# Kernel optimization log

Measured on AMD Instinct MI355X. Metric: run time of the kernel, lower is better.

Reference implementation:

```python
import jax, jax.numpy as jnp
import numpy as np

M, K, N = 4096, 4096, 4096

def setup_inputs() -> dict:
    key = jax.random.key(0)
    k1, k2, k3 = jax.random.split(key, 3)
    a = jax.random.randint(k1, (M, K), 0, 127, dtype=jnp.int32)
    b = jax.random.randint(k2, (K, N), 0, 127, dtype=jnp.int32)
    scale = jax.random.uniform(k3, (N,), dtype=jnp.float32)
    return {"a": a, "b": b, "scale": scale}

def reference(a, b, scale):
    a8 = a.astype(jnp.int8)
    b8 = b.astype(jnp.int8)
    acc = jnp.matmul(a8, b8, preferred_element_type=jnp.int32)  # [M, N] int32
    # fused per-column (per-output-channel) dequantization scale
    return acc.astype(jnp.float32) * scale[None, :]  # [M, N] float32
```

## Files before the change

### kernel.cpp

```cpp
#include <hip/hip_runtime.h>
#include <stdint.h>

#define M_DIM 4096
#define K_DIM 4096
#define N_DIM 4096

typedef int v4i __attribute__((ext_vector_type(4)));
typedef int int32x4 __attribute__((ext_vector_type(4)));

__device__ __forceinline__ void gload_lds16(const void* g, void* l) {
    __builtin_amdgcn_global_load_lds(
        (const __attribute__((address_space(1))) uint32_t*)g,
        (__attribute__((address_space(3))) uint32_t*)l, 16, 0, 0);
}

__global__ void pack_ab_kernel(const int* __restrict__ a, char* __restrict__ a8,
                               const int* __restrict__ b, char* __restrict__ b8t) {
    __shared__ char tile[64][68];
    if (blockIdx.x < 2048) {
        int idx = blockIdx.x * 256 + threadIdx.x;
        const int stride = 2048 * 256;
        const int total4 = M_DIM * K_DIM / 4;
        for (int i = idx; i < total4; i += stride) {
            int32x4 v = ((const int32x4*)a)[i];
            uint32_t p = (uint32_t)(v.x & 0xff) | ((uint32_t)(v.y & 0xff) << 8) |
                         ((uint32_t)(v.z & 0xff) << 16) | ((uint32_t)(v.w & 0xff) << 24);
            ((uint32_t*)a8)[i] = p;
        }
    } else {
        int bid2 = blockIdx.x - 2048;
        int n0 = (bid2 & 63) * 64;
        int k0 = (bid2 >> 6) * 64;
        int tx = threadIdx.x & 63;
        int ty = threadIdx.x >> 6;
#pragma unroll
        for (int kk = 0; kk < 64; kk += 4) {
            tile[kk + ty][tx] = (char)b[(size_t)(k0 + kk + ty) * N_DIM + n0 + tx];
        }
        __syncthreads();
        int td = threadIdx.x & 15;
        int tn = threadIdx.x >> 4;
#pragma unroll
        for (int nn0 = 0; nn0 < 64; nn0 += 16) {
            int nn = nn0 + tn;
            uint32_t p = (uint32_t)(uint8_t)tile[td * 4 + 0][nn] |
                         ((uint32_t)(uint8_t)tile[td * 4 + 1][nn] << 8) |
                         ((uint32_t)(uint8_t)tile[td * 4 + 2][nn] << 16) |
                         ((uint32_t)(uint8_t)tile[td * 4 + 3][nn] << 24);
            *(uint32_t*)&b8t[(size_t)(n0 + nn) * K_DIM + k0 + td * 4] = p;
        }
    }
}

#define BM 256
#define BN 256
#define KTILES (K_DIM / 64)

#define BAR __builtin_amdgcn_s_barrier()
#define WAIT_VM4 asm volatile("s_waitcnt vmcnt(4)" ::: "memory")
#define WAIT_VM0 asm volatile("s_waitcnt vmcnt(0)" ::: "memory")
#define WAIT_LGKM0 asm volatile("s_waitcnt lgkmcnt(0)" ::: "memory")

#define RD_FRAGS(RA, RB)                                                                \
    _Pragma("unroll") for (int i_ = 0; i_ < 8; ++i_)                                    \
        RA[i_] = *(const v4i*)(lds + nxt + aOff + i_ * 1024);                           \
    _Pragma("unroll") for (int j_ = 0; j_ < 4; ++j_)                                    \
        RB[j_] = *(const v4i*)(lds + nxt + bOff + j_ * 1024);

#define SGB_HINT                                                                        \
    _Pragma("unroll") for (int g_ = 0; g_ < 12; ++g_) {                                 \
        __builtin_amdgcn_sched_group_barrier(0x100, 1, 0);               \
        __builtin_amdgcn_sched_group_barrier(0x008, 2, 0);                  \
    }                                                                                   \
    __builtin_amdgcn_sched_group_barrier(0x008, 8, 0);

#define MFMA32(AF, BF)                                                                  \
    __builtin_amdgcn_s_setprio(1);                                                      \
    _Pragma("unroll") for (int i_ = 0; i_ < 8; ++i_)                                    \
    _Pragma("unroll") for (int j_ = 0; j_ < 4; ++j_)                                    \
        acc[i_][j_] = __builtin_amdgcn_mfma_i32_16x16x64_i8(AF[i_], BF[j_],             \
                                                            acc[i_][j_], 0, 0, 0);     \
    __builtin_amdgcn_s_setprio(0);

#define WINDOW(w, RA, RB, MA, MB)                                                       \
    {                                                                                   \
        stage((w) + 2, stg);                                                            \
        WAIT_VM4;                                                                       \
        BAR;                                                                            \
        RD_FRAGS(RA, RB);                                                               \
        SGB_HINT;                                                                       \
        MFMA32(MA, MB);                                                                 \
        WAIT_LGKM0;                                                                     \
        int t_ = cur; cur = nxt; nxt = stg; stg = t_;                                   \
    }

__global__ __launch_bounds__(512, 2) void gemm_i8_pp(const char* __restrict__ A8,
                                                     const char* __restrict__ B8T,
                                                     const float* __restrict__ scale,
                                                     float* __restrict__ out) {
    __shared__ char lds[98304];

    int tid = threadIdx.x;
    int wave = tid >> 6;
    int lane = tid & 63;
    int wr = wave >> 2;
    int wc = wave & 3;
    int l15 = lane & 15;

    int bid = blockIdx.x;
    int swz = (bid & 7) * 32 + (bid >> 3);
    int bm = swz >> 4;
    int bn = swz & 15;

    int rA = tid >> 2;
    int cc = ((tid & 3) ^ ((tid >> 3) & 3)) << 4;
    const char* aSrc = A8 + (size_t)(bm * BM + rA) * K_DIM + cc;
    const char* bSrc = B8T + (size_t)(bn * BN + rA) * K_DIM + cc;

    int slot = (((lane >> 4) ^ ((lane >> 1) & 3)) << 4);
    int aOff = wr * 8192 + l15 * 64 + slot;
    int bOff = 16384 + wc * 4096 + l15 * 64 + slot;

    v4i acc[8][4];
#pragma unroll
    for (int i = 0; i < 8; ++i)
#pragma unroll
        for (int j = 0; j < 4; ++j) acc[i][j] = (v4i){0, 0, 0, 0};

    auto stage = [&](int w, int bo) {
        const char* sa = aSrc + (size_t)w * 64;
        const char* sb = bSrc + (size_t)w * 64;
        char* da = (char*)lds + bo + wave * 1024;
        char* db = da + 16384;
        gload_lds16(sa, da);
        gload_lds16(sa + (size_t)128 * K_DIM, da + 8192);
        gload_lds16(sb, db);
        gload_lds16(sb + (size_t)128 * K_DIM, db + 8192);
    };

    stage(0, 0);
    stage(1, 32768);
    WAIT_VM4;
    BAR;

    int cur = 0, nxt = 32768, stg = 65536;
    v4i pA[8], pB[4], qA[8], qB[4];
    {
#pragma unroll
        for (int i = 0; i < 8; ++i) pA[i] = *(const v4i*)(lds + cur + aOff + i * 1024);
#pragma unroll
        for (int j = 0; j < 4; ++j) pB[j] = *(const v4i*)(lds + cur + bOff + j * 1024);
    }

    for (int kt = 0; kt < KTILES - 2; kt += 2) {
        WINDOW(kt, qA, qB, pA, pB);
        WINDOW(kt + 1, pA, pB, qA, qB);
    }

    WAIT_VM0;
    BAR;
    RD_FRAGS(qA, qB);
    MFMA32(pA, pB);
    MFMA32(qA, qB);

    size_t orow0 = (size_t)bm * BM + wr * 128 + (lane >> 4) * 4;
    int ocol0 = bn * BN + wc * 64 + l15;
#pragma unroll
    for (int j = 0; j < 4; ++j) {
        int col = ocol0 + j * 16;
        float s = scale[col];
#pragma unroll
        for (int i = 0; i < 8; ++i) {
            size_t row = orow0 + (size_t)i * 16;
#pragma unroll
            for (int r = 0; r < 4; ++r) {
                out[(row + r) * N_DIM + col] = (float)acc[i][j][r] * s;
            }
        }
    }
}

#define FBM 128
#define FBN 128
#define FBK 64

__global__ __launch_bounds__(256) void gemm_i8_fused_kernel(const int* __restrict__ a,
                                                            const int* __restrict__ b,
                                                            const float* __restrict__ scale,
                                                            float* __restrict__ out) {
    __shared__ char As[FBM * FBK];
    __shared__ char Bs[FBN * FBK];

    int tid = threadIdx.x;
    int wave = tid >> 6;
    int lane = tid & 63;

    int nwg = gridDim.x;
    int cpx = nwg >> 3;
    int bid = blockIdx.x;
    int swz = (bid & 7) * cpx + (bid >> 3);
    int bm = swz >> 5;
    int bn = swz & 31;

    int f0 = tid * 16;
    int m0 = f0 >> 6;
    int k0 = f0 & 63;

    int nn = tid & 127;
    int kh = tid >> 7;

    int wr = wave >> 1;
    int wc = wave & 1;
    int lrow = lane & 15;
    int kgrp = (lane >> 4) * 16;

    v4i acc[4][4];
#pragma unroll
    for (int i = 0; i < 4; ++i)
#pragma unroll
        for (int j = 0; j < 4; ++j) acc[i][j] = (v4i){0, 0, 0, 0};

    const int kTiles = K_DIM / FBK;
    for (int kt = 0; kt < kTiles; ++kt) {
        __syncthreads();
#pragma unroll
        for (int r = 0; r < 2; ++r) {
            const int* src = a + (size_t)(bm * FBM + m0 + r * 64) * K_DIM + kt * FBK + k0;
            uint32_t pk[4];
#pragma unroll
            for (int q = 0; q < 4; ++q) {
                int32x4 v = *(const int32x4*)(src + q * 4);
                pk[q] = (uint32_t)(v.x & 0xff) | ((uint32_t)(v.y & 0xff) << 8) |
                        ((uint32_t)(v.z & 0xff) << 16) | ((uint32_t)(v.w & 0xff) << 24);
            }
            *(v4i*)&As[f0 + r * 4096] = (v4i){(int)pk[0], (int)pk[1], (int)pk[2], (int)pk[3]};
        }
#pragma unroll
        for (int d = 0; d < 8; ++d) {
            uint32_t p = 0;
#pragma unroll
            for (int i = 0; i < 4; ++i) {
                int kk = kt * FBK + kh * 32 + d * 4 + i;
                p |= (uint32_t)(b[(size_t)kk * N_DIM + bn * FBN + nn] & 0xff) << (8 * i);
            }
            *(uint32_t*)&Bs[nn * 64 + kh * 32 + d * 4] = p;
        }
        __syncthreads();

        v4i aF[4], bF[4];
#pragma unroll
        for (int i = 0; i < 4; ++i)
            aF[i] = *(const v4i*)&As[(wr * 64 + i * 16 + lrow) * FBK + kgrp];
#pragma unroll
        for (int j = 0; j < 4; ++j)
            bF[j] = *(const v4i*)&Bs[(wc * 64 + j * 16 + lrow) * FBK + kgrp];
#pragma unroll
        for (int i = 0; i < 4; ++i)
#pragma unroll
            for (int j = 0; j < 4; ++j)
                acc[i][j] = __builtin_amdgcn_mfma_i32_16x16x64_i8(aF[i], bF[j], acc[i][j], 0, 0, 0);
    }

    size_t orow0 = (size_t)bm * FBM + wr * 64;
    int ocol0 = bn * FBN + wc * 64;
#pragma unroll
    for (int j = 0; j < 4; ++j) {
        int col = ocol0 + j * 16 + lrow;
        float s = scale[col];
#pragma unroll
        for (int i = 0; i < 4; ++i) {
            size_t row = orow0 + i * 16 + (lane >> 4) * 4;
#pragma unroll
            for (int r = 0; r < 4; ++r) {
                out[(row + r) * N_DIM + col] = (float)acc[i][j][r] * s;
            }
        }
    }
}

extern "C" void kernel_launch(void* const* d_in, const int* in_sizes, int n_in,
                              void* d_out, int out_size, void* d_ws, size_t ws_size,
                              hipStream_t stream) {
    const int* a = (const int*)d_in[0];
    const int* b = (const int*)d_in[1];
    const float* scale = (const float*)d_in[2];
    float* out = (float*)d_out;

    size_t need = (size_t)M_DIM * K_DIM + (size_t)K_DIM * N_DIM;
    if (ws_size >= need) {
        char* a8 = (char*)d_ws;
        char* b8t = a8 + (size_t)M_DIM * K_DIM;
        pack_ab_kernel<<<2048 + 4096, 256, 0, stream>>>(a, a8, b, b8t);
        gemm_i8_pp<<<256, 512, 0, stream>>>(a8, b8t, scale, out);
    } else {
        gemm_i8_fused_kernel<<<1024, 256, 0, stream>>>(a, b, scale, out);
    }
}
```

Before: 93.30 us.

## Load B fragments directly from global into registers, stage only A in LDS

B operand fragments now go straight from global memory into registers one k-tile ahead, so B no longer passes through LDS. This halves the LDS footprint and removes the LDS reads for B. The wait counts and scheduling hints are retuned to match, and the block swizzle swaps bm and bn. In exchange, each B fragment is a 16-byte strided load straight from HBM/L2 with no LDS reuse across the waves that share the same columns, which may raise global traffic and latency exposure.

```diff
diff --git a/kernel.cpp b/kernel.cpp
--- a/kernel.cpp
+++ b/kernel.cpp
@@ -57,20 +57,20 @@
 #define KTILES (K_DIM / 64)
 
 #define BAR __builtin_amdgcn_s_barrier()
+#define WAIT_VM6 asm volatile("s_waitcnt vmcnt(6)" ::: "memory")
 #define WAIT_VM4 asm volatile("s_waitcnt vmcnt(4)" ::: "memory")
+#define WAIT_VM2 asm volatile("s_waitcnt vmcnt(2)" ::: "memory")
 #define WAIT_VM0 asm volatile("s_waitcnt vmcnt(0)" ::: "memory")
 #define WAIT_LGKM0 asm volatile("s_waitcnt lgkmcnt(0)" ::: "memory")
 
-#define RD_FRAGS(RA, RB)                                                                \
+#define RD_A(RA)                                                                        \
     _Pragma("unroll") for (int i_ = 0; i_ < 8; ++i_)                                    \
-        RA[i_] = *(const v4i*)(lds + nxt + aOff + i_ * 1024);                           \
-    _Pragma("unroll") for (int j_ = 0; j_ < 4; ++j_)                                    \
-        RB[j_] = *(const v4i*)(lds + nxt + bOff + j_ * 1024);
+        RA[i_] = *(const v4i*)(lds + nxt + aOff + i_ * 1024);
 
 #define SGB_HINT                                                                        \
-    _Pragma("unroll") for (int g_ = 0; g_ < 12; ++g_) {                                 \
+    _Pragma("unroll") for (int g_ = 0; g_ < 8; ++g_) {                                  \
         __builtin_amdgcn_sched_group_barrier(0x100, 1, 0);               \
-        __builtin_amdgcn_sched_group_barrier(0x008, 2, 0);                  \
+        __builtin_amdgcn_sched_group_barrier(0x008, 3, 0);                  \
     }                                                                                   \
     __builtin_amdgcn_sched_group_barrier(0x008, 8, 0);
 
@@ -82,23 +82,24 @@
                                                             acc[i_][j_], 0, 0, 0);     \
     __builtin_amdgcn_s_setprio(0);
 
-#define WINDOW(w, RA, RB, MA, MB)                                                       \
+#define WINDOW(w, LA, LB, UA, UB)                                                       \
     {                                                                                   \
+        loadB((w) + 1, LB);                                                             \
         stage((w) + 2, stg);                                                            \
-        WAIT_VM4;                                                                       \
+        WAIT_VM6;                                                                       \
         BAR;                                                                            \
-        RD_FRAGS(RA, RB);                                                               \
+        RD_A(LA);                                                                       \
         SGB_HINT;                                                                       \
-        MFMA32(MA, MB);                                                                 \
+        MFMA32(UA, UB);                                                                 \
         WAIT_LGKM0;                                                                     \
         int t_ = cur; cur = nxt; nxt = stg; stg = t_;                                   \
     }
 
-__global__ __launch_bounds__(512, 2) void gemm_i8_pp(const char* __restrict__ A8,
+__global__ __launch_bounds__(512, 2) void gemm_i8_bd(const char* __restrict__ A8,
                                                      const char* __restrict__ B8T,
                                                      const float* __restrict__ scale,
                                                      float* __restrict__ out) {
-    __shared__ char lds[98304];
+    __shared__ char lds[49152];
 
     int tid = threadIdx.x;
     int wave = tid >> 6;
@@ -109,17 +110,18 @@
 
     int bid = blockIdx.x;
     int swz = (bid & 7) * 32 + (bid >> 3);
-    int bm = swz >> 4;
-    int bn = swz & 15;
+    int bm = swz & 15;
+    int bn = swz >> 4;
 
     int rA = tid >> 2;
     int cc = ((tid & 3) ^ ((tid >> 3) & 3)) << 4;
     const char* aSrc = A8 + (size_t)(bm * BM + rA) * K_DIM + cc;
-    const char* bSrc = B8T + (size_t)(bn * BN + rA) * K_DIM + cc;
+
+    const char* bFragSrc =
+        B8T + (size_t)(bn * BN + wc * 64 + l15) * K_DIM + ((lane >> 4) << 4);
 
     int slot = (((lane >> 4) ^ ((lane >> 1) & 3)) << 4);
     int aOff = wr * 8192 + l15 * 64 + slot;
-    int bOff = 16384 + wc * 4096 + l15 * 64 + slot;
 
     v4i acc[8][4];
 #pragma unroll
@@ -129,38 +131,39 @@
 
     auto stage = [&](int w, int bo) {
         const char* sa = aSrc + (size_t)w * 64;
-        const char* sb = bSrc + (size_t)w * 64;
         char* da = (char*)lds + bo + wave * 1024;
-        char* db = da + 16384;
         gload_lds16(sa, da);
         gload_lds16(sa + (size_t)128 * K_DIM, da + 8192);
-        gload_lds16(sb, db);
-        gload_lds16(sb + (size_t)128 * K_DIM, db + 8192);
     };
+    auto loadB = [&](int w, v4i* dst) {
+#pragma unroll
+        for (int j = 0; j < 4; ++j)
+            dst[j] = *(const v4i*)(bFragSrc + (size_t)j * 16 * K_DIM + (size_t)w * 64);
+    };
+
+    v4i pA[8], qA[8], pB[4], qB[4];
 
     stage(0, 0);
-    stage(1, 32768);
-    WAIT_VM4;
+    loadB(0, pB);
+    stage(1, 16384);
+    WAIT_VM2;
     BAR;
-
-    int cur = 0, nxt = 32768, stg = 65536;
-    v4i pA[8], pB[4], qA[8], qB[4];
-    {
-#pragma unroll
-        for (int i = 0; i < 8; ++i) pA[i] = *(const v4i*)(lds + cur + aOff + i * 1024);
-#pragma unroll
-        for (int j = 0; j < 4; ++j) pB[j] = *(const v4i*)(lds + cur + bOff + j * 1024);
-    }
+#pragma unroll
+    for (int i = 0; i < 8; ++i) pA[i] = *(const v4i*)(lds + 0 + aOff + i * 1024);
+
+    int cur = 0, nxt = 16384, stg = 32768;
 
     for (int kt = 0; kt < KTILES - 2; kt += 2) {
         WINDOW(kt, qA, qB, pA, pB);
         WINDOW(kt + 1, pA, pB, qA, qB);
     }
 
+    loadB(63, qB);
+    WAIT_VM4;
+    BAR;
+    RD_A(qA);
+    MFMA32(pA, pB);
     WAIT_VM0;
-    BAR;
-    RD_FRAGS(qA, qB);
-    MFMA32(pA, pB);
     MFMA32(qA, qB);
 
     size_t orow0 = (size_t)bm * BM + wr * 128 + (lane >> 4) * 4;
@@ -291,7 +294,7 @@
         char* a8 = (char*)d_ws;
         char* b8t = a8 + (size_t)M_DIM * K_DIM;
         pack_ab_kernel<<<2048 + 4096, 256, 0, stream>>>(a, a8, b, b8t);
-        gemm_i8_pp<<<256, 512, 0, stream>>>(a8, b8t, scale, out);
+        gemm_i8_bd<<<256, 512, 0, stream>>>(a8, b8t, scale, out);
     } else {
         gemm_i8_fused_kernel<<<1024, 256, 0, stream>>>(a, b, scale, out);
     }
```

Result: slower. 115.6 us (+23.9%).

## Switch int8 GEMM to 128-wide K tiles with double-buffered LDS

Applied to the files above, without the earlier changes.

Replaces the triple-buffered 64-wide K pipeline with a double-buffered pipeline over 128-wide K tiles, using 128 KB of LDS. Each window issues eight global-to-LDS loads and 64 MFMAs, which halves the number of barriers and loop iterations per K. The LDS swizzle changes to an 8-chunk XOR on 128-byte rows, and the fragment reads are interleaved with MFMAs through a new sched_group_barrier pattern. The trade-off is less prefetch depth: only one tile is in flight instead of two, and a barrier has to be added before each stage. The larger LDS footprint may also cut residency to one block per CU instead of two.

```diff
diff --git a/kernel.cpp b/kernel.cpp
--- a/kernel.cpp
+++ b/kernel.cpp
@@ -54,25 +54,19 @@
 
 #define BM 256
 #define BN 256
-#define KTILES (K_DIM / 64)
+#define KTILES (K_DIM / 128)
 
 #define BAR __builtin_amdgcn_s_barrier()
-#define WAIT_VM4 asm volatile("s_waitcnt vmcnt(4)" ::: "memory")
+#define WAIT_VM8 asm volatile("s_waitcnt vmcnt(8)" ::: "memory")
 #define WAIT_VM0 asm volatile("s_waitcnt vmcnt(0)" ::: "memory")
-#define WAIT_LGKM0 asm volatile("s_waitcnt lgkmcnt(0)" ::: "memory")
-
-#define RD_FRAGS(RA, RB)                                                                \
-    _Pragma("unroll") for (int i_ = 0; i_ < 8; ++i_)                                    \
-        RA[i_] = *(const v4i*)(lds + nxt + aOff + i_ * 1024);                           \
-    _Pragma("unroll") for (int j_ = 0; j_ < 4; ++j_)                                    \
-        RB[j_] = *(const v4i*)(lds + nxt + bOff + j_ * 1024);
-
-#define SGB_HINT                                                                        \
-    _Pragma("unroll") for (int g_ = 0; g_ < 12; ++g_) {                                 \
-        __builtin_amdgcn_sched_group_barrier(0x100, 1, 0);               \
-        __builtin_amdgcn_sched_group_barrier(0x008, 2, 0);                  \
+
+#define SGB_W128                                                                        \
+    __builtin_amdgcn_sched_group_barrier(0x100, 5, 0);                                  \
+    _Pragma("unroll") for (int g_ = 0; g_ < 19; ++g_) {                                 \
+        __builtin_amdgcn_sched_group_barrier(0x100, 1, 0);                              \
+        __builtin_amdgcn_sched_group_barrier(0x008, 3, 0);                              \
     }                                                                                   \
-    __builtin_amdgcn_sched_group_barrier(0x008, 8, 0);
+    __builtin_amdgcn_sched_group_barrier(0x008, 7, 0);
 
 #define MFMA32(AF, BF)                                                                  \
     __builtin_amdgcn_s_setprio(1);                                                      \
@@ -82,23 +76,26 @@
                                                             acc[i_][j_], 0, 0, 0);     \
     __builtin_amdgcn_s_setprio(0);
 
-#define WINDOW(w, RA, RB, MA, MB)                                                       \
+#define COMPUTE_WIN(cur)                                                                \
     {                                                                                   \
-        stage((w) + 2, stg);                                                            \
-        WAIT_VM4;                                                                       \
-        BAR;                                                                            \
-        RD_FRAGS(RA, RB);                                                               \
-        SGB_HINT;                                                                       \
-        MFMA32(MA, MB);                                                                 \
-        WAIT_LGKM0;                                                                     \
-        int t_ = cur; cur = nxt; nxt = stg; stg = t_;                                   \
-    }
-
-__global__ __launch_bounds__(512, 2) void gemm_i8_pp(const char* __restrict__ A8,
-                                                     const char* __restrict__ B8T,
-                                                     const float* __restrict__ scale,
-                                                     float* __restrict__ out) {
-    __shared__ char lds[98304];
+        _Pragma("unroll") for (int j_ = 0; j_ < 4; ++j_)                                \
+            fB0[j_] = *(const v4i*)(lds + (cur) + bBase + j_ * 2048);                   \
+        _Pragma("unroll") for (int i_ = 0; i_ < 8; ++i_)                                \
+            fA0[i_] = *(const v4i*)(lds + (cur) + aBase + i_ * 2048);                   \
+        _Pragma("unroll") for (int j_ = 0; j_ < 4; ++j_)                                \
+            fB1[j_] = *(const v4i*)(lds + (cur) + ((bBase + j_ * 2048) ^ 64));          \
+        _Pragma("unroll") for (int i_ = 0; i_ < 8; ++i_)                                \
+            fA1[i_] = *(const v4i*)(lds + (cur) + ((aBase + i_ * 2048) ^ 64));          \
+        SGB_W128;                                                                       \
+        MFMA32(fA0, fB0);                                                               \
+        MFMA32(fA1, fB1);                                                               \
+    }
+
+__global__ __launch_bounds__(512, 2) void gemm_i8_w128(const char* __restrict__ A8,
+                                                       const char* __restrict__ B8T,
+                                                       const float* __restrict__ scale,
+                                                       float* __restrict__ out) {
+    __shared__ char lds[131072];
 
     int tid = threadIdx.x;
     int wave = tid >> 6;
@@ -106,20 +103,21 @@
     int wr = wave >> 2;
     int wc = wave & 3;
     int l15 = lane & 15;
+    int q = lane >> 4;
 
     int bid = blockIdx.x;
     int swz = (bid & 7) * 32 + (bid >> 3);
     int bm = swz >> 4;
     int bn = swz & 15;
 
-    int rA = tid >> 2;
-    int cc = ((tid & 3) ^ ((tid >> 3) & 3)) << 4;
-    const char* aSrc = A8 + (size_t)(bm * BM + rA) * K_DIM + cc;
-    const char* bSrc = B8T + (size_t)(bn * BN + rA) * K_DIM + cc;
-
-    int slot = (((lane >> 4) ^ ((lane >> 1) & 3)) << 4);
-    int aOff = wr * 8192 + l15 * 64 + slot;
-    int bOff = 16384 + wc * 4096 + l15 * 64 + slot;
+    int sRow = tid >> 3;
+    int sCh = ((tid & 7) ^ (sRow & 7)) << 4;
+    const char* aSrc = A8 + (size_t)(bm * BM + sRow) * K_DIM + sCh;
+    const char* bSrc = B8T + (size_t)(bn * BN + sRow) * K_DIM + sCh;
+
+    int slot0 = ((q ^ (l15 & 7)) << 4);
+    int aBase = (wr * 128 + l15) * 128 + slot0;
+    int bBase = 32768 + (wc * 64 + l15) * 128 + slot0;
 
     v4i acc[8][4];
 #pragma unroll
@@ -128,40 +126,35 @@
         for (int j = 0; j < 4; ++j) acc[i][j] = (v4i){0, 0, 0, 0};
 
     auto stage = [&](int w, int bo) {
-        const char* sa = aSrc + (size_t)w * 64;
-        const char* sb = bSrc + (size_t)w * 64;
+        const char* sa = aSrc + (size_t)w * 128;
+        const char* sb = bSrc + (size_t)w * 128;
         char* da = (char*)lds + bo + wave * 1024;
-        char* db = da + 16384;
-        gload_lds16(sa, da);
-        gload_lds16(sa + (size_t)128 * K_DIM, da + 8192);
-        gload_lds16(sb, db);
-        gload_lds16(sb + (size_t)128 * K_DIM, db + 8192);
+#pragma unroll
+        for (int r = 0; r < 4; ++r) {
+            gload_lds16(sa + (size_t)r * 64 * K_DIM, da + r * 8192);
+            gload_lds16(sb + (size_t)r * 64 * K_DIM, da + 32768 + r * 8192);
+        }
     };
 
+    v4i fA0[8], fB0[4], fA1[8], fB1[4];
+
     stage(0, 0);
-    stage(1, 32768);
-    WAIT_VM4;
-    BAR;
-
-    int cur = 0, nxt = 32768, stg = 65536;
-    v4i pA[8], pB[4], qA[8], qB[4];
+
+    for (int w = 0; w < KTILES - 1; ++w) {
+        int cur = (w & 1) << 16;
+        BAR;
+        stage(w + 1, cur ^ 65536);
+        WAIT_VM8;
+        BAR;
+        COMPUTE_WIN(cur);
+    }
+
     {
-#pragma unroll
-        for (int i = 0; i < 8; ++i) pA[i] = *(const v4i*)(lds + cur + aOff + i * 1024);
-#pragma unroll
-        for (int j = 0; j < 4; ++j) pB[j] = *(const v4i*)(lds + cur + bOff + j * 1024);
-    }
-
-    for (int kt = 0; kt < KTILES - 2; kt += 2) {
-        WINDOW(kt, qA, qB, pA, pB);
-        WINDOW(kt + 1, pA, pB, qA, qB);
-    }
-
-    WAIT_VM0;
-    BAR;
-    RD_FRAGS(qA, qB);
-    MFMA32(pA, pB);
-    MFMA32(qA, qB);
+        int cur = ((KTILES - 1) & 1) << 16;
+        WAIT_VM0;
+        BAR;
+        COMPUTE_WIN(cur);
+    }
 
     size_t orow0 = (size_t)bm * BM + wr * 128 + (lane >> 4) * 4;
     int ocol0 = bn * BN + wc * 64 + l15;
@@ -291,7 +284,7 @@
         char* a8 = (char*)d_ws;
         char* b8t = a8 + (size_t)M_DIM * K_DIM;
         pack_ab_kernel<<<2048 + 4096, 256, 0, stream>>>(a, a8, b, b8t);
-        gemm_i8_pp<<<256, 512, 0, stream>>>(a8, b8t, scale, out);
+        gemm_i8_w128<<<256, 512, 0, stream>>>(a8, b8t, scale, out);
     } else {
         gemm_i8_fused_kernel<<<1024, 256, 0, stream>>>(a, b, scale, out);
     }
```

Result: slower. 97.05 us (+4.0%).

## Use 4 fat waves per block with 128x128 per-wave tiles instead of 8

Applied to the files above, without the earlier changes.

Restructures the int8 GEMM block from 8 waves (each 128x64 output) to 4 waves (each 128x128 output), doubling per-wave accumulators and B fragments and the MFMAs per window. Each thread now issues 8 global-to-LDS loads per stage, with the wait count and scheduling hints adjusted to match, and the priority toggling is dropped. The aim is more register-level reuse of LDS fragments and fewer LDS reads per MFMA. In exchange, registers per wave rise sharply and fewer waves are resident to hide latency.

```diff
diff --git a/kernel.cpp b/kernel.cpp
--- a/kernel.cpp
+++ b/kernel.cpp
@@ -57,54 +57,51 @@
 #define KTILES (K_DIM / 64)
 
 #define BAR __builtin_amdgcn_s_barrier()
-#define WAIT_VM4 asm volatile("s_waitcnt vmcnt(4)" ::: "memory")
+#define WAIT_VM8 asm volatile("s_waitcnt vmcnt(8)" ::: "memory")
 #define WAIT_VM0 asm volatile("s_waitcnt vmcnt(0)" ::: "memory")
 #define WAIT_LGKM0 asm volatile("s_waitcnt lgkmcnt(0)" ::: "memory")
 
 #define RD_FRAGS(RA, RB)                                                                \
     _Pragma("unroll") for (int i_ = 0; i_ < 8; ++i_)                                    \
         RA[i_] = *(const v4i*)(lds + nxt + aOff + i_ * 1024);                           \
-    _Pragma("unroll") for (int j_ = 0; j_ < 4; ++j_)                                    \
+    _Pragma("unroll") for (int j_ = 0; j_ < 8; ++j_)                                    \
         RB[j_] = *(const v4i*)(lds + nxt + bOff + j_ * 1024);
 
 #define SGB_HINT                                                                        \
-    _Pragma("unroll") for (int g_ = 0; g_ < 12; ++g_) {                                 \
+    _Pragma("unroll") for (int g_ = 0; g_ < 16; ++g_) {                                 \
         __builtin_amdgcn_sched_group_barrier(0x100, 1, 0);               \
-        __builtin_amdgcn_sched_group_barrier(0x008, 2, 0);                  \
-    }                                                                                   \
-    __builtin_amdgcn_sched_group_barrier(0x008, 8, 0);
-
-#define MFMA32(AF, BF)                                                                  \
-    __builtin_amdgcn_s_setprio(1);                                                      \
+        __builtin_amdgcn_sched_group_barrier(0x008, 4, 0);                  \
+    }
+
+#define MFMA64(AF, BF)                                                                  \
     _Pragma("unroll") for (int i_ = 0; i_ < 8; ++i_)                                    \
-    _Pragma("unroll") for (int j_ = 0; j_ < 4; ++j_)                                    \
+    _Pragma("unroll") for (int j_ = 0; j_ < 8; ++j_)                                    \
         acc[i_][j_] = __builtin_amdgcn_mfma_i32_16x16x64_i8(AF[i_], BF[j_],             \
-                                                            acc[i_][j_], 0, 0, 0);     \
-    __builtin_amdgcn_s_setprio(0);
-
-#define WINDOW(w, RA, RB, MA, MB)                                                       \
+                                                            acc[i_][j_], 0, 0, 0);
+
+#define WINDOW(w, LA, LB, UA, UB)                                                       \
     {                                                                                   \
         stage((w) + 2, stg);                                                            \
-        WAIT_VM4;                                                                       \
+        WAIT_VM8;                                                                       \
         BAR;                                                                            \
-        RD_FRAGS(RA, RB);                                                               \
+        RD_FRAGS(LA, LB);                                                               \
         SGB_HINT;                                                                       \
-        MFMA32(MA, MB);                                                                 \
+        MFMA64(UA, UB);                                                                 \
         WAIT_LGKM0;                                                                     \
         int t_ = cur; cur = nxt; nxt = stg; stg = t_;                                   \
     }
 
-__global__ __launch_bounds__(512, 2) void gemm_i8_pp(const char* __restrict__ A8,
-                                                     const char* __restrict__ B8T,
-                                                     const float* __restrict__ scale,
-                                                     float* __restrict__ out) {
+__global__ __launch_bounds__(256, 1) void gemm_i8_fat(const char* __restrict__ A8,
+                                                      const char* __restrict__ B8T,
+                                                      const float* __restrict__ scale,
+                                                      float* __restrict__ out) {
     __shared__ char lds[98304];
 
     int tid = threadIdx.x;
     int wave = tid >> 6;
     int lane = tid & 63;
-    int wr = wave >> 2;
-    int wc = wave & 3;
+    int wr = wave >> 1;
+    int wc = wave & 1;
     int l15 = lane & 15;
 
     int bid = blockIdx.x;
@@ -112,45 +109,43 @@
     int bm = swz >> 4;
     int bn = swz & 15;
 
-    int rA = tid >> 2;
+    int sRow = tid >> 2;
     int cc = ((tid & 3) ^ ((tid >> 3) & 3)) << 4;
-    const char* aSrc = A8 + (size_t)(bm * BM + rA) * K_DIM + cc;
-    const char* bSrc = B8T + (size_t)(bn * BN + rA) * K_DIM + cc;
+    const char* aSrc = A8 + (size_t)(bm * BM + sRow) * K_DIM + cc;
+    const char* bSrc = B8T + (size_t)(bn * BN + sRow) * K_DIM + cc;
 
     int slot = (((lane >> 4) ^ ((lane >> 1) & 3)) << 4);
     int aOff = wr * 8192 + l15 * 64 + slot;
-    int bOff = 16384 + wc * 4096 + l15 * 64 + slot;
-
-    v4i acc[8][4];
+    int bOff = 16384 + wc * 8192 + l15 * 64 + slot;
+
+    v4i acc[8][8];
 #pragma unroll
     for (int i = 0; i < 8; ++i)
 #pragma unroll
-        for (int j = 0; j < 4; ++j) acc[i][j] = (v4i){0, 0, 0, 0};
+        for (int j = 0; j < 8; ++j) acc[i][j] = (v4i){0, 0, 0, 0};
 
     auto stage = [&](int w, int bo) {
         const char* sa = aSrc + (size_t)w * 64;
         const char* sb = bSrc + (size_t)w * 64;
         char* da = (char*)lds + bo + wave * 1024;
-        char* db = da + 16384;
-        gload_lds16(sa, da);
-        gload_lds16(sa + (size_t)128 * K_DIM, da + 8192);
-        gload_lds16(sb, db);
-        gload_lds16(sb + (size_t)128 * K_DIM, db + 8192);
+#pragma unroll
+        for (int r = 0; r < 4; ++r) {
+            gload_lds16(sa + (size_t)r * 64 * K_DIM, da + r * 4096);
+            gload_lds16(sb + (size_t)r * 64 * K_DIM, da + 16384 + r * 4096);
+        }
     };
 
     stage(0, 0);
     stage(1, 32768);
-    WAIT_VM4;
+    WAIT_VM8;
     BAR;
 
     int cur = 0, nxt = 32768, stg = 65536;
-    v4i pA[8], pB[4], qA[8], qB[4];
-    {
-#pragma unroll
-        for (int i = 0; i < 8; ++i) pA[i] = *(const v4i*)(lds + cur + aOff + i * 1024);
-#pragma unroll
-        for (int j = 0; j < 4; ++j) pB[j] = *(const v4i*)(lds + cur + bOff + j * 1024);
-    }
+    v4i pA[8], pB[8], qA[8], qB[8];
+#pragma unroll
+    for (int i = 0; i < 8; ++i) pA[i] = *(const v4i*)(lds + cur + aOff + i * 1024);
+#pragma unroll
+    for (int j = 0; j < 8; ++j) pB[j] = *(const v4i*)(lds + cur + bOff + j * 1024);
 
     for (int kt = 0; kt < KTILES - 2; kt += 2) {
         WINDOW(kt, qA, qB, pA, pB);
@@ -160,13 +155,14 @@
     WAIT_VM0;
     BAR;
     RD_FRAGS(qA, qB);
-    MFMA32(pA, pB);
-    MFMA32(qA, qB);
+    MFMA64(pA, pB);
+    WAIT_LGKM0;
+    MFMA64(qA, qB);
 
     size_t orow0 = (size_t)bm * BM + wr * 128 + (lane >> 4) * 4;
-    int ocol0 = bn * BN + wc * 64 + l15;
-#pragma unroll
-    for (int j = 0; j < 4; ++j) {
+    int ocol0 = bn * BN + wc * 128 + l15;
+#pragma unroll
+    for (int j = 0; j < 8; ++j) {
         int col = ocol0 + j * 16;
         float s = scale[col];
 #pragma unroll
@@ -291,7 +287,7 @@
         char* a8 = (char*)d_ws;
         char* b8t = a8 + (size_t)M_DIM * K_DIM;
         pack_ab_kernel<<<2048 + 4096, 256, 0, stream>>>(a, a8, b, b8t);
-        gemm_i8_pp<<<256, 512, 0, stream>>>(a8, b8t, scale, out);
+        gemm_i8_fat<<<256, 256, 0, stream>>>(a8, b8t, scale, out);
     } else {
         gemm_i8_fused_kernel<<<1024, 256, 0, stream>>>(a, b, scale, out);
     }
```

Result: slower. 115.5 us (+23.8%).
